# Kernel tuning notes

Hardware: AMD Instinct MI355X
Metric: run time of the kernel (lower is better)

## Reference

```python
import jax, jax.numpy as jnp
import numpy as np

DIM = 1024
HEADS = 16
HEAD_DIM = DIM // HEADS


def setup_inputs() -> dict:
    key = jax.random.key(0)
    ks = jax.random.split(key, 5)
    B, N = 4, 2048
    x = jax.random.normal(ks[0], (B, N, DIM), dtype=jnp.float32)
    # nn.Linear default init scale ~ 1/sqrt(fan_in)
    s = 1.0 / np.sqrt(DIM)
    W_qkv = jax.random.uniform(ks[1], (DIM, 3 * DIM), minval=-s, maxval=s, dtype=jnp.float32)
    b_qkv = jax.random.uniform(ks[2], (3 * DIM,), minval=-s, maxval=s, dtype=jnp.float32)
    W_proj = jax.random.uniform(ks[3], (DIM, DIM), minval=-s, maxval=s, dtype=jnp.float32)
    b_proj = jax.random.uniform(ks[4], (DIM,), minval=-s, maxval=s, dtype=jnp.float32)
    return {"x": x, "W_qkv": W_qkv, "b_qkv": b_qkv, "W_proj": W_proj, "b_proj": b_proj}


def reference(x, W_qkv, b_qkv, W_proj, b_proj):
    B, N, C = x.shape
    qkv = x @ W_qkv + b_qkv                      # [B, N, 3C]
    qkv = qkv.reshape(B, N, 3, HEADS, HEAD_DIM)
    q = jnp.transpose(qkv[:, :, 0], (0, 2, 1, 3))  # [B, H, N, D]
    k = jnp.transpose(qkv[:, :, 1], (0, 2, 1, 3))
    v = jnp.transpose(qkv[:, :, 2], (0, 2, 1, 3))
    scale = 1.0 / np.sqrt(HEAD_DIM)
    scores = jnp.einsum('bhqd,bhkd->bhqk', q, k) * scale  # [B, H, N, N]
    attn = jax.nn.softmax(scores, axis=-1)
    out = jnp.einsum('bhqk,bhkd->bhqd', attn, v)           # [B, H, N, D]
    out = jnp.transpose(out, (0, 2, 1, 3)).reshape(B, N, C)
    return out @ W_proj + b_proj
```

## Files before the change

kernel.cpp:

```cpp
#include <hip/hip_runtime.h>

typedef __attribute__((ext_vector_type(2)))  float  f32x2;
typedef __attribute__((ext_vector_type(4)))  float  f32x4;
typedef __attribute__((ext_vector_type(16))) float  f32x16;
typedef __attribute__((ext_vector_type(8)))  short  short8;
typedef __attribute__((ext_vector_type(4)))  unsigned int u32x4;
typedef __attribute__((ext_vector_type(2)))  unsigned int uint2v;

#define MFMA16 __builtin_amdgcn_mfma_f32_16x16x32_bf16
#define MFMA32 __builtin_amdgcn_mfma_f32_32x32x16_bf16

static __device__ __forceinline__ unsigned short f2bf(float f){
  union { float f; unsigned u; } v; v.f = f;
  unsigned r = v.u + 0x7fffu + ((v.u >> 16) & 1u);
  return (unsigned short)(r >> 16);
}

static __device__ __forceinline__ unsigned cvtpk(float a, float b){
  unsigned r;
  asm("v_cvt_pk_bf16_f32 %0, %1, %2" : "=v"(r) : "v"(a), "v"(b));
  return r;
}

static __device__ __forceinline__ void plswap(unsigned &a, unsigned &b){
  asm("v_permlane32_swap_b32 %0, %1" : "+v"(a), "+v"(b));
}

static __device__ __forceinline__ float max3f(float a, float b, float c){
  return fmaxf(fmaxf(a, b), c);
}

typedef __attribute__((address_space(1))) void gvoid_t;
typedef __attribute__((address_space(3))) void lvoid_t;

static __device__ __forceinline__ void gll16(const unsigned short* g, unsigned short* l){
  __builtin_amdgcn_global_load_lds((gvoid_t*)g, (lvoid_t*)l, 16, 0, 0);
}


__global__ __launch_bounds__(256) void k_convert(const float* __restrict__ x,
                                                 unsigned short* __restrict__ xb){
  __shared__ __align__(16) unsigned short sm[16384];
  const int mblk = blockIdx.x >> 4, kt = blockIdx.x & 15;
  const int t = threadIdx.x;
  const int l16 = t & 15, rg = t >> 4;
  #pragma unroll
  for (int p = 0; p < 16; p++){
    int row = p * 16 + rg;
    f32x4 v = *(const f32x4*)&x[(size_t)(mblk*256 + row) * 1024 + kt*64 + l16*4];
    uint2v u; u[0] = cvtpk(v[0], v[1]); u[1] = cvtpk(v[2], v[3]);
    int g = l16 >> 1;
    *(uint2v*)&sm[row*64 + ((g ^ (row & 7)) << 3) + (l16 & 1)*4] = u;
  }
  __syncthreads();
  size_t obase = (size_t)((mblk*16 + kt)*2) * 8192;
  #pragma unroll
  for (int i = 0; i < 8; i++){
    int o = i * 256 + t;
    int kh = o >> 10, rem = o & 1023;
    int band = rem >> 6, cc = (rem >> 4) & 3, ri = rem & 15;
    int r = band*16 + ri, g = kh*4 + cc;
    short8 vv = *(const short8*)&sm[r*64 + ((g ^ (r & 7)) << 3)];
    *(short8*)&xb[obase + (size_t)kh*8192 + rem*8] = vv;
  }
}

__global__ __launch_bounds__(256) void k_transpose(const float* __restrict__ W,
                                                   unsigned short* __restrict__ Wt,
                                                   int K, int N){
  __shared__ float tile[32][33];
  int n0 = blockIdx.x * 32, k0 = blockIdx.y * 32;
  int tx = threadIdx.x, ty = threadIdx.y;
  #pragma unroll
  for (int r = 0; r < 4; r++)
    tile[ty + 8*r][tx] = W[(size_t)(k0 + ty + 8*r) * N + n0 + tx];
  __syncthreads();
  #pragma unroll
  for (int r = 0; r < 4; r++){
    int nn = ty + 8*r;
    int n = n0 + nn, k = k0 + tx;
    int kt = k >> 6, kh = (k >> 5) & 1, cc = (k >> 3) & 3, ke = k & 7;
    int nblk = n >> 8, band = (n & 255) >> 4, ri = n & 15;
    Wt[(size_t)(((nblk*16 + kt)*2 + kh)) * 8192 + band*512 + cc*128 + ri*8 + ke] =
        f2bf(tile[tx][nn]);
  }
}

#define GSYNC3 { __builtin_amdgcn_sched_barrier(0);                        \
                 asm volatile("s_waitcnt vmcnt(3)" ::: "memory");          \
                 __builtin_amdgcn_s_barrier();                             \
                 __builtin_amdgcn_sched_barrier(0); }
#define GSYNC0 { __builtin_amdgcn_sched_barrier(0);                        \
                 asm volatile("s_waitcnt vmcnt(0)" ::: "memory");          \
                 __builtin_amdgcn_s_barrier();                             \
                 __builtin_amdgcn_sched_barrier(0); }

template<int MODE>
__global__ __launch_bounds__(512, 2) void k_gemm(const unsigned short* __restrict__ A,
                                                 const unsigned short* __restrict__ Bt,
                                                 const float* __restrict__ bias,
                                                 void* __restrict__ outp,
                                                 int NT){
  __shared__ __align__(16) unsigned short lds[49152];
  const int t = threadIdx.x, w = t >> 6, l = t & 63;
  const int wr = w >> 2, wc = w & 3;
  const int bx = blockIdx.x, by = blockIdx.y;
  const int mblk = bx >> 1, mhalf = bx & 1;

  const unsigned short* Ab = A + (size_t)mblk*262144 + mhalf*4096 + t*8;
  const unsigned short* Bb = Bt + (size_t)by*262144 + t*8;

  f32x4 acc[4][4];
  #pragma unroll
  for (int i = 0; i < 4; i++)
    #pragma unroll
    for (int j = 0; j < 4; j++)
      acc[i][j] = (f32x4){0.f, 0.f, 0.f, 0.f};

#define GSTAGE(c2, ks, ktile) {                                                   \
    gll16(Ab + (size_t)(ktile)*16384 + (ks)*8192, &lds[(c2)*8192 + (ks)*4096 + t*8]); \
    gll16(Bb + (size_t)(ktile)*16384 + (ks)*8192, &lds[16384 + (c2)*16384 + (ks)*8192 + t*8]); \
    gll16(Bb + (size_t)(ktile)*16384 + (ks)*8192 + 4096, &lds[16384 + (c2)*16384 + (ks)*8192 + 4096 + t*8]); }

#define GPHASE(c2, ks) {                                                          \
    short8 af[4], bfr[4];                                                         \
    const int aoff = (c2)*8192 + (ks)*4096 + wr*2048 + l*8;                       \
    const int boff = 16384 + (c2)*16384 + (ks)*8192 + wc*2048 + l*8;              \
    _Pragma("unroll")                                                             \
    for (int i = 0; i < 4; i++) af[i]  = *(const short8*)&lds[aoff + i*512];      \
    _Pragma("unroll")                                                             \
    for (int j = 0; j < 4; j++) bfr[j] = *(const short8*)&lds[boff + j*512];      \
    __builtin_amdgcn_s_setprio(1);                                                \
    _Pragma("unroll")                                                             \
    for (int i = 0; i < 4; i++)                                                   \
      _Pragma("unroll")                                                           \
      for (int j = 0; j < 4; j++)                                                 \
        acc[i][j] = MFMA16(af[i], bfr[j], acc[i][j], 0, 0, 0);                    \
    __builtin_amdgcn_s_setprio(0); }

  GSTAGE(0, 0, 0);
  GSTAGE(0, 1, 0);
  GSYNC3;

  for (int kt2 = 0; kt2 < NT; kt2++){
    const int c = kt2 & 1, n2 = c ^ 1;
    const bool pre = kt2 < NT - 1;
    if (pre) GSTAGE(n2, 0, kt2 + 1);
    GPHASE(c, 0);
    if (pre) GSYNC3 else GSYNC0;
    if (pre) GSTAGE(n2, 1, kt2 + 1);
    GPHASE(c, 1);
    if (pre) GSYNC3;
  }

  if (MODE == 0){
    unsigned short* qg = (unsigned short*)outp;
    unsigned short* kg = qg + (size_t)8388608;
    unsigned short* vg = kg + (size_t)8388608;
    const int which = by >> 2;
    const int lrow = l & 15;
    #pragma unroll
    for (int j = 0; j < 4; j++){
      int col = by*256 + wc*64 + j*16 + lrow;
      float bi = bias[col];
      int cc = col & 1023;
      int h = cc >> 6;
      int d = j*16 + lrow;
      if (which == 2){
        int db = d >> 5, dd = d & 31;
        #pragma unroll
        for (int i = 0; i < 4; i++){
          int nn = bx*128 + wr*64 + i*16 + (l >> 4)*4;
          int b = nn >> 11, key = nn & 2047;
          size_t idx = (size_t)(key >> 6)*4096 + (size_t)(((key >> 4) & 3)*2 + db)*512
                     + (((key >> 3) & 1)*32 + dd)*8 + (key & 7);
          uint2v u;
          u[0] = cvtpk(acc[i][j][0] + bi, acc[i][j][1] + bi);
          u[1] = cvtpk(acc[i][j][2] + bi, acc[i][j][3] + bi);
          *(uint2v*)&vg[(size_t)(b*16 + h)*131072 + idx] = u;
        }
      } else {
        unsigned short* dst = which ? kg : qg;
        float scale = which ? 1.0f : 0.18033688011f;
        int dsub = (d >> 4)*512 + ((d >> 3) & 1)*256 + (d & 7);
        #pragma unroll
        for (int i = 0; i < 4; i++)
          #pragma unroll
          for (int reg = 0; reg < 4; reg++){
            int nn = bx*128 + wr*64 + i*16 + (l >> 4)*4 + reg;
            int b = nn >> 11, row = nn & 2047;
            dst[(size_t)(b*16 + h)*131072 + (size_t)(row >> 5)*2048 + dsub + (row & 31)*8] =
                f2bf((acc[i][j][reg] + bi) * scale);
          }
      }
    }
  } else {
    float* out = (float*)outp;
    #pragma unroll
    for (int i = 0; i < 4; i++)
      #pragma unroll
      for (int reg = 0; reg < 4; reg++){
        int row = bx*128 + wr*64 + i*16 + (l >> 4)*4 + reg;
        #pragma unroll
        for (int j = 0; j < 4; j++){
          int col = by*256 + wc*64 + j*16 + (l & 15);
          out[(size_t)row * 1024 + col] = acc[i][j][reg] + bias[col];
        }
      }
  }
#undef GSTAGE
#undef GPHASE
}

__global__ __launch_bounds__(256, 4) void k_attn(const unsigned short* __restrict__ Qg,
                                                 const unsigned short* __restrict__ Kg,
                                                 const unsigned short* __restrict__ Vg,
                                                 unsigned short* __restrict__ aout){
  __shared__ __align__(16) unsigned short lds[16384];

  const int t = threadIdx.x, w = t >> 6, l = t & 63;
  const int hi = l >> 5, q31 = l & 31;
  const int d0 = blockIdx.x;
  const int xcd = d0 & 7, jj = d0 >> 3;
  const int bh = xcd + 8*(jj >> 4);
  const int bx = jj & 15;

  const unsigned short* Qp = Qg + (size_t)bh*131072 + (size_t)bx*8192;
  const unsigned short* Kp = Kg + (size_t)bh*131072;
  const unsigned short* Vp = Vg + (size_t)bh*131072;

  #pragma unroll
  for (int i = 0; i < 4; i++){ int c = i*256 + t; gll16(Qp + c*8, &lds[c*8]); }
  __syncthreads();
  short8 qf[4];
  #pragma unroll
  for (int ds = 0; ds < 4; ds++)
    qf[ds] = *(const short8*)&lds[(w*4 + ds)*512 + l*8];
  __syncthreads();

  #pragma unroll
  for (int i = 0; i < 2; i++){
    int c = i*256 + t;
    gll16(Kp + c*8, &lds[c*8]);
    gll16(Vp + c*8, &lds[4096 + c*8]);
  }
  __syncthreads();

  f32x16 oacc0, oacc1;
  #pragma unroll
  for (int i = 0; i < 16; i++){ oacc0[i] = 0.f; oacc1[i] = 0.f; }
  float m = -1e30f, lsum = 0.f;

  for (int kt = 0; kt < 32; kt++){
    const int cb = (kt & 1) * 8192;
    if (kt < 31){
      const int nb = cb ^ 8192;
      #pragma unroll
      for (int i = 0; i < 2; i++){
        int c = i*256 + t;
        gll16(Kp + (size_t)(kt + 1)*4096 + c*8, &lds[nb + c*8]);
        gll16(Vp + (size_t)(kt + 1)*4096 + c*8, &lds[nb + 4096 + c*8]);
      }
    }

    f32x16 sA, sB;
    #pragma unroll
    for (int i = 0; i < 16; i++){ sA[i] = 0.f; sB[i] = 0.f; }
    __builtin_amdgcn_s_setprio(1);
    #pragma unroll
    for (int ds = 0; ds < 4; ds++){
      short8 kfA = *(const short8*)&lds[cb + ds*512 + l*8];
      short8 kfB = *(const short8*)&lds[cb + 2048 + ds*512 + l*8];
      sA = MFMA32(kfA, qf[ds], sA, 0, 0, 0);
      sB = MFMA32(kfB, qf[ds], sB, 0, 0, 0);
    }
    __builtin_amdgcn_s_setprio(0);

    float mx = max3f(
        max3f(max3f(sA[0], sA[1], sA[2]),  max3f(sA[3], sA[4], sA[5]),
              max3f(sA[6], sA[7], sA[8])),
        max3f(max3f(sA[9], sA[10], sA[11]), max3f(sA[12], sA[13], sA[14]),
              max3f(sA[15], sB[0], sB[1])),
        max3f(max3f(max3f(sB[2], sB[3], sB[4]),  max3f(sB[5], sB[6], sB[7]),
                    max3f(sB[8], sB[9], sB[10])),
              max3f(sB[11], sB[12], sB[13]),
              fmaxf(sB[14], sB[15])));
    mx = fmaxf(mx, __shfl_xor(mx, 32));
    if (!__all(mx - m <= 8.0f)){
      float mn = fmaxf(m, mx);
      float sf = __builtin_amdgcn_exp2f(m - mn);
      m = mn; lsum *= sf;
      #pragma unroll
      for (int i = 0; i < 16; i++){ oacc0[i] *= sf; oacc1[i] *= sf; }
    }
    f32x2 mm; mm[0] = m; mm[1] = m;
    f32x2 a2[8], b2[8];
    #pragma unroll
    for (int j = 0; j < 8; j++){
      f32x2 ta; ta[0] = sA[2*j]; ta[1] = sA[2*j+1];
      f32x2 tb; tb[0] = sB[2*j]; tb[1] = sB[2*j+1];
      a2[j] = ta - mm;
      b2[j] = tb - mm;
    }
    #pragma unroll
    for (int j = 0; j < 8; j++){
      a2[j][0] = __builtin_amdgcn_exp2f(a2[j][0]);
      a2[j][1] = __builtin_amdgcn_exp2f(a2[j][1]);
      b2[j][0] = __builtin_amdgcn_exp2f(b2[j][0]);
      b2[j][1] = __builtin_amdgcn_exp2f(b2[j][1]);
    }
    f32x2 s2 = ((a2[0] + a2[1]) + (a2[2] + a2[3])) + ((a2[4] + a2[5]) + (a2[6] + a2[7]))
             + ((b2[0] + b2[1]) + (b2[2] + b2[3])) + ((b2[4] + b2[5]) + (b2[6] + b2[7]));
    float rs = s2[0] + s2[1];
    rs += __shfl_xor(rs, 32);
    lsum += rs;

    unsigned wA[8], wB[8];
    #pragma unroll
    for (int j = 0; j < 8; j++){
      wA[j] = cvtpk(a2[j][0], a2[j][1]);
      wB[j] = cvtpk(b2[j][0], b2[j][1]);
    }
    u32x4 pf[4];
    { unsigned a = wA[0], b = wA[2]; plswap(a, b); pf[0][0] = a; pf[0][2] = b; }
    { unsigned a = wA[1], b = wA[3]; plswap(a, b); pf[0][1] = a; pf[0][3] = b; }
    { unsigned a = wA[4], b = wA[6]; plswap(a, b); pf[1][0] = a; pf[1][2] = b; }
    { unsigned a = wA[5], b = wA[7]; plswap(a, b); pf[1][1] = a; pf[1][3] = b; }
    { unsigned a = wB[0], b = wB[2]; plswap(a, b); pf[2][0] = a; pf[2][2] = b; }
    { unsigned a = wB[1], b = wB[3]; plswap(a, b); pf[2][1] = a; pf[2][3] = b; }
    { unsigned a = wB[4], b = wB[6]; plswap(a, b); pf[3][0] = a; pf[3][2] = b; }
    { unsigned a = wB[5], b = wB[7]; plswap(a, b); pf[3][1] = a; pf[3][3] = b; }

    __builtin_amdgcn_s_setprio(1);
    #pragma unroll
    for (int ks = 0; ks < 4; ks++){
      short8 pfr;
      *(u32x4*)&pfr = pf[ks];
      short8 vf0 = *(const short8*)&lds[cb + 4096 + (ks*2 + 0)*512 + l*8];
      short8 vf1 = *(const short8*)&lds[cb + 4096 + (ks*2 + 1)*512 + l*8];
      oacc0 = MFMA32(vf0, pfr, oacc0, 0, 0, 0);
      oacc1 = MFMA32(vf1, pfr, oacc1, 0, 0, 0);
    }
    __builtin_amdgcn_s_setprio(0);

    __syncthreads();
  }

  {
    float inv = 1.0f / lsum;
    int qrow = w*32 + q31;
    #pragma unroll
    for (int j = 0; j < 8; j++){
      int dd0 = 8*(j >> 1) + 2*(j & 1) + 4*hi;
      unsigned u0 = cvtpk(oacc0[2*j] * inv, oacc0[2*j+1] * inv);
      *(unsigned*)&lds[qrow*64 + (((dd0 >> 3) ^ (qrow & 7)) << 3) + (dd0 & 7)] = u0;
      int dd1 = dd0 + 32;
      unsigned u1 = cvtpk(oacc1[2*j] * inv, oacc1[2*j+1] * inv);
      *(unsigned*)&lds[qrow*64 + (((dd1 >> 3) ^ (qrow & 7)) << 3) + (dd1 & 7)] = u1;
    }
  }
  __syncthreads();
  {
    int mblk16 = (bh >> 4)*8 + (bx >> 1);
    int h = bh & 15;
    int bandbase = 8*(bx & 1);
    #pragma unroll
    for (int i = 0; i < 4; i++){
      int idx = i*256 + t;
      int kh = idx >> 9, band_l = (idx >> 6) & 7, cc = (idx >> 4) & 3, ri = idx & 15;
      int r = band_l*16 + ri, g = kh*4 + cc;
      short8 vv = *(const short8*)&lds[r*64 + ((g ^ (r & 7)) << 3)];
      size_t chunk = (size_t)((mblk16*16 + h)*2 + kh);
      *(short8*)&aout[chunk*8192 + (size_t)(bandbase + band_l)*512 + cc*128 + ri*8] = vv;
    }
  }
}

extern "C" void kernel_launch(void* const* d_in, const int* in_sizes, int n_in,
                              void* d_out, int out_size, void* d_ws, size_t ws_size,
                              hipStream_t stream){
  const float* x     = (const float*)d_in[0];
  const float* Wqkv  = (const float*)d_in[1];
  const float* bqkv  = (const float*)d_in[2];
  const float* Wproj = (const float*)d_in[3];
  const float* bproj = (const float*)d_in[4];

  unsigned short* ws   = (unsigned short*)d_ws;
  unsigned short* xb   = ws;
  unsigned short* Wqt  = ws + (size_t)8192 * 1024;
  unsigned short* Wpt  = Wqt + (size_t)3072 * 1024;
  unsigned short* qkvb = Wpt + (size_t)1024 * 1024;

  k_convert<<<512, 256, 0, stream>>>(x, xb);
  k_transpose<<<dim3(96, 32), dim3(32, 8), 0, stream>>>(Wqkv, Wqt, 1024, 3072);
  k_transpose<<<dim3(32, 32), dim3(32, 8), 0, stream>>>(Wproj, Wpt, 1024, 1024);
  k_gemm<0><<<dim3(64, 12), 512, 0, stream>>>(xb, Wqt, bqkv, qkvb, 16);
  k_attn<<<1024, 256, 0, stream>>>(qkvb, qkvb + (size_t)8388608,
                                   qkvb + (size_t)16777216, xb);
  k_gemm<1><<<dim3(64, 4), 512, 0, stream>>>(xb, Wpt, bproj, (void*)d_out, 16);
}
```

Baseline: 188.3 us.

## Software-pipeline attention by overlapping previous tile's PV MFMA with current QK

```diff
diff --git a/kernel.cpp b/kernel.cpp
--- a/kernel.cpp
+++ b/kernel.cpp
@@ -216,7 +216,7 @@
                                                  const unsigned short* __restrict__ Kg,
                                                  const unsigned short* __restrict__ Vg,
                                                  unsigned short* __restrict__ aout){
-  __shared__ __align__(16) unsigned short lds[16384];
+  __shared__ __align__(16) unsigned short lds[20480];
 
   const int t = threadIdx.x, w = t >> 6, l = t & 63;
   const int hi = l >> 5, q31 = l & 31;
@@ -236,13 +236,18 @@
   #pragma unroll
   for (int ds = 0; ds < 4; ds++)
     qf[ds] = *(const short8*)&lds[(w*4 + ds)*512 + l*8];
+  {
+    short8 z8 = {0,0,0,0,0,0,0,0};
+    *(short8*)&lds[16384 + t*16]     = z8;
+    *(short8*)&lds[16384 + t*16 + 8] = z8;
+  }
   __syncthreads();
 
   #pragma unroll
   for (int i = 0; i < 2; i++){
     int c = i*256 + t;
     gll16(Kp + c*8, &lds[c*8]);
-    gll16(Vp + c*8, &lds[4096 + c*8]);
+    gll16(Vp + c*8, &lds[8192 + c*8]);
   }
   __syncthreads();
 
@@ -250,29 +255,44 @@
   #pragma unroll
   for (int i = 0; i < 16; i++){ oacc0[i] = 0.f; oacc1[i] = 0.f; }
   float m = -1e30f, lsum = 0.f;
+  u32x4 pfp[4];
+  #pragma unroll
+  for (int ks = 0; ks < 4; ks++){ pfp[ks][0]=0u; pfp[ks][1]=0u; pfp[ks][2]=0u; pfp[ks][3]=0u; }
+  int s0 = 0, s1 = 1, s2 = 2;
 
   for (int kt = 0; kt < 32; kt++){
-    const int cb = (kt & 1) * 8192;
+    const int cbk = (kt & 1) * 4096;
     if (kt < 31){
-      const int nb = cb ^ 8192;
+      const int nbk = cbk ^ 4096;
+      const int nv  = 8192 + s1*4096;
       #pragma unroll
       for (int i = 0; i < 2; i++){
         int c = i*256 + t;
-        gll16(Kp + (size_t)(kt + 1)*4096 + c*8, &lds[nb + c*8]);
-        gll16(Vp + (size_t)(kt + 1)*4096 + c*8, &lds[nb + 4096 + c*8]);
+        gll16(Kp + (size_t)(kt + 1)*4096 + c*8, &lds[nbk + c*8]);
+        gll16(Vp + (size_t)(kt + 1)*4096 + c*8, &lds[nv + c*8]);
       }
     }
 
     f32x16 sA, sB;
     #pragma unroll
     for (int i = 0; i < 16; i++){ sA[i] = 0.f; sB[i] = 0.f; }
+    const int pvb = 8192 + s2*4096;
     __builtin_amdgcn_s_setprio(1);
     #pragma unroll
     for (int ds = 0; ds < 4; ds++){
-      short8 kfA = *(const short8*)&lds[cb + ds*512 + l*8];
-      short8 kfB = *(const short8*)&lds[cb + 2048 + ds*512 + l*8];
+      short8 kfA = *(const short8*)&lds[cbk + ds*512 + l*8];
+      short8 kfB = *(const short8*)&lds[cbk + 2048 + ds*512 + l*8];
       sA = MFMA32(kfA, qf[ds], sA, 0, 0, 0);
       sB = MFMA32(kfB, qf[ds], sB, 0, 0, 0);
+    }
+    #pragma unroll
+    for (int ks = 0; ks < 4; ks++){
+      short8 pfr;
+      *(u32x4*)&pfr = pfp[ks];
+      short8 vf0 = *(const short8*)&lds[pvb + (ks*2 + 0)*512 + l*8];
+      short8 vf1 = *(const short8*)&lds[pvb + (ks*2 + 1)*512 + l*8];
+      oacc0 = MFMA32(vf0, pfr, oacc0, 0, 0, 0);
+      oacc1 = MFMA32(vf1, pfr, oacc1, 0, 0, 0);
     }
     __builtin_amdgcn_s_setprio(0);
 
@@ -309,9 +329,9 @@
       b2[j][0] = __builtin_amdgcn_exp2f(b2[j][0]);
       b2[j][1] = __builtin_amdgcn_exp2f(b2[j][1]);
     }
-    f32x2 s2 = ((a2[0] + a2[1]) + (a2[2] + a2[3])) + ((a2[4] + a2[5]) + (a2[6] + a2[7]))
-             + ((b2[0] + b2[1]) + (b2[2] + b2[3])) + ((b2[4] + b2[5]) + (b2[6] + b2[7]));
-    float rs = s2[0] + s2[1];
+    f32x2 s2v = ((a2[0] + a2[1]) + (a2[2] + a2[3])) + ((a2[4] + a2[5]) + (a2[6] + a2[7]))
+              + ((b2[0] + b2[1]) + (b2[2] + b2[3])) + ((b2[4] + b2[5]) + (b2[6] + b2[7]));
+    float rs = s2v[0] + s2v[1];
     rs += __shfl_xor(rs, 32);
     lsum += rs;
 
@@ -321,29 +341,32 @@
       wA[j] = cvtpk(a2[j][0], a2[j][1]);
       wB[j] = cvtpk(b2[j][0], b2[j][1]);
     }
-    u32x4 pf[4];
-    { unsigned a = wA[0], b = wA[2]; plswap(a, b); pf[0][0] = a; pf[0][2] = b; }
-    { unsigned a = wA[1], b = wA[3]; plswap(a, b); pf[0][1] = a; pf[0][3] = b; }
-    { unsigned a = wA[4], b = wA[6]; plswap(a, b); pf[1][0] = a; pf[1][2] = b; }
-    { unsigned a = wA[5], b = wA[7]; plswap(a, b); pf[1][1] = a; pf[1][3] = b; }
-    { unsigned a = wB[0], b = wB[2]; plswap(a, b); pf[2][0] = a; pf[2][2] = b; }
-    { unsigned a = wB[1], b = wB[3]; plswap(a, b); pf[2][1] = a; pf[2][3] = b; }
-    { unsigned a = wB[4], b = wB[6]; plswap(a, b); pf[3][0] = a; pf[3][2] = b; }
-    { unsigned a = wB[5], b = wB[7]; plswap(a, b); pf[3][1] = a; pf[3][3] = b; }
-
+    { unsigned a = wA[0], b = wA[2]; plswap(a, b); pfp[0][0] = a; pfp[0][2] = b; }
+    { unsigned a = wA[1], b = wA[3]; plswap(a, b); pfp[0][1] = a; pfp[0][3] = b; }
+    { unsigned a = wA[4], b = wA[6]; plswap(a, b); pfp[1][0] = a; pfp[1][2] = b; }
+    { unsigned a = wA[5], b = wA[7]; plswap(a, b); pfp[1][1] = a; pfp[1][3] = b; }
+    { unsigned a = wB[0], b = wB[2]; plswap(a, b); pfp[2][0] = a; pfp[2][2] = b; }
+    { unsigned a = wB[1], b = wB[3]; plswap(a, b); pfp[2][1] = a; pfp[2][3] = b; }
+    { unsigned a = wB[4], b = wB[6]; plswap(a, b); pfp[3][0] = a; pfp[3][2] = b; }
+    { unsigned a = wB[5], b = wB[7]; plswap(a, b); pfp[3][1] = a; pfp[3][3] = b; }
+
+    __syncthreads();
+    int tmp = s2; s2 = s0; s0 = s1; s1 = tmp;
+  }
+
+  {
+    const int pvb = 8192 + s2*4096;
     __builtin_amdgcn_s_setprio(1);
     #pragma unroll
     for (int ks = 0; ks < 4; ks++){
       short8 pfr;
-      *(u32x4*)&pfr = pf[ks];
-      short8 vf0 = *(const short8*)&lds[cb + 4096 + (ks*2 + 0)*512 + l*8];
-      short8 vf1 = *(const short8*)&lds[cb + 4096 + (ks*2 + 1)*512 + l*8];
+      *(u32x4*)&pfr = pfp[ks];
+      short8 vf0 = *(const short8*)&lds[pvb + (ks*2 + 0)*512 + l*8];
+      short8 vf1 = *(const short8*)&lds[pvb + (ks*2 + 1)*512 + l*8];
       oacc0 = MFMA32(vf0, pfr, oacc0, 0, 0, 0);
       oacc1 = MFMA32(vf1, pfr, oacc1, 0, 0, 0);
     }
     __builtin_amdgcn_s_setprio(0);
-
-    __syncthreads();
   }
 
   {
```

Result: no change. 188.2 us (-0.0%).
